# Kernel tuning notes

Hardware: AMD Instinct MI355X
Metric: run time of the kernel (lower is better)

The kernel has to match this reference:

```python
import jax, jax.numpy as jnp
import numpy as np

HID = 1024
NH = 4
DK = 256   # head_qk_dim
DV = 512   # head_v_dim
C = 64     # chunk size (fla default)
EPS = 1e-5
GLN = 16.0  # gate_logit_normalizer


def _xavier(key, shape, gain=2 ** (-2.5)):
    fan_in, fan_out = shape
    lim = gain * np.sqrt(6.0 / (fan_in + fan_out))
    return jax.random.uniform(key, shape, jnp.float32, -lim, lim)


def setup_inputs() -> dict:
    key = jax.random.key(0)
    ks = jax.random.split(key, 8)
    x = jax.random.normal(ks[0], (4, 2048, HID), jnp.float32)
    Wq = _xavier(ks[1], (HID, NH * DK))
    Wk = _xavier(ks[2], (HID, NH * DK))
    Wv = _xavier(ks[3], (HID, NH * DV))
    Wg = _xavier(ks[4], (HID, NH * DV))
    Wgk = _xavier(ks[5], (HID, NH))
    bgk = jnp.zeros((NH,), jnp.float32)
    Wo = _xavier(ks[6], (NH * DV, HID))
    gnorm_w = jnp.ones((DV,), jnp.float32)
    return {"x": x, "Wq": Wq, "Wk": Wk, "Wv": Wv, "Wg": Wg,
            "Wgk": Wgk, "bgk": bgk, "Wo": Wo, "gnorm_w": gnorm_w}


def _chunk_simple_gla(q, k, v, g):
    # q,k: [b,h,n,dk]; v: [b,h,n,dv]; g: [b,h,n] per-head scalar log-decay
    B, H, N, dk = q.shape
    dv = v.shape[-1]
    nc = N // C
    scale = dk ** -0.5
    q = q.reshape(B, H, nc, C, dk) * scale
    k = k.reshape(B, H, nc, C, dk)
    v = v.reshape(B, H, nc, C, dv)
    g = g.reshape(B, H, nc, C)
    gc = jnp.cumsum(g, axis=-1)          # inclusive within-chunk cumulative decay
    gt = gc[..., -1]                     # total chunk decay [b,h,nc]

    # intra-chunk: o[t] += sum_{s<=t} exp(gc_t - gc_s) (q_t.k_s) v_s
    dec = gc[..., :, None] - gc[..., None, :]              # [b,h,nc,C,C]
    mask = jnp.tril(jnp.ones((C, C), bool))
    A = jnp.einsum('bhntd,bhnsd->bhnts', q, k)
    A = A * jnp.where(mask, jnp.exp(jnp.where(mask, dec, 0.0)), 0.0)
    o_intra = jnp.einsum('bhnts,bhnsd->bhntd', A, v)

    # inter-chunk: carry state S [b,h,dk,dv] across chunks
    qs = jnp.moveaxis(q, 2, 0)
    ks_ = jnp.moveaxis(k, 2, 0)
    vs = jnp.moveaxis(v, 2, 0)
    gcs = jnp.moveaxis(gc, 2, 0)
    gts = jnp.moveaxis(gt, 2, 0)
    S0 = jnp.zeros((B, H, dk, dv), q.dtype)

    def step(S, inp):
        qc, kc, vc, gcc, gtc = inp
        o_int = jnp.einsum('bhtd,bhde->bhte', qc * jnp.exp(gcc)[..., None], S)
        kd = kc * jnp.exp(gtc[..., None] - gcc)[..., None]
        S = jnp.exp(gtc)[..., None, None] * S + jnp.einsum('bhtd,bhte->bhde', kd, vc)
        return S, o_int

    _, o_inter = jax.lax.scan(step, S0, (qs, ks_, vs, gcs, gts))
    o = o_intra + jnp.moveaxis(o_inter, 0, 2)
    return o.reshape(B, H, N, dv)


def reference(x, Wq, Wk, Wv, Wg, Wgk, bgk, Wo, gnorm_w):
    B, N, _ = x.shape
    q = (x @ Wq).reshape(B, N, NH, DK).transpose(0, 2, 1, 3)
    k = (x @ Wk).reshape(B, N, NH, DK).transpose(0, 2, 1, 3)
    v = (x @ Wv).reshape(B, N, NH, DV).transpose(0, 2, 1, 3)
    gk = (x @ Wgk + bgk).transpose(0, 2, 1)          # [b,h,n]
    gk = jax.nn.log_sigmoid(gk) / GLN
    o = _chunk_simple_gla(q, k, v, gk)               # [b,h,n,dv]
    o = o.transpose(0, 2, 1, 3)                      # [b,n,h,dv]
    g = (x @ Wg).reshape(B, N, NH, DV)
    # FusedRMSNormSwishGate: RMSNorm(o) * swish(g)
    on = o * jax.lax.rsqrt(jnp.mean(o * o, axis=-1, keepdims=True) + EPS) * gnorm_w
    o = on * (g * jax.nn.sigmoid(g))
    o = o.reshape(B, N, NH * DV)
    return o @ Wo
```

## Files before the change

### kernel.cpp

```cpp
#include <hip/hip_runtime.h>

constexpr int B_  = 4;
constexpr int N_  = 2048;
constexpr int HID_ = 1024;
constexpr int NH_ = 4;
constexpr int DK_ = 256;
constexpr int DV_ = 512;
constexpr int C_  = 64;
constexpr int NC_ = 32;
constexpr int M_  = B_ * N_;
constexpr int NSEG_ = 4;
constexpr int CSEG_ = NC_ / NSEG_;
constexpr int QW_ = 6144;

using ushort_t = unsigned short;
typedef __attribute__((ext_vector_type(8))) short bf16x8;
typedef __attribute__((ext_vector_type(4))) float f32x4;

__device__ __forceinline__ ushort_t f2bf(float f) {
  union { float fv; unsigned u; } v; v.fv = f;
  unsigned r = v.u + 0x7FFFu + ((v.u >> 16) & 1u);
  return (ushort_t)(r >> 16);
}
__device__ __forceinline__ float bf2f(ushort_t u) {
  union { unsigned u; float f; } v; v.u = ((unsigned)u) << 16; return v.f;
}

__device__ __forceinline__ void gload_lds16(const void* g, void* l) {
  __builtin_amdgcn_global_load_lds(
      (const __attribute__((address_space(1))) unsigned int*)g,
      (__attribute__((address_space(3))) unsigned int*)l, 16, 0, 0);
}

__device__ __forceinline__ f32x4 mfma16(bf16x8 a, bf16x8 b, f32x4 c) {
  return __builtin_amdgcn_mfma_f32_16x16x32_bf16(a, b, c, 0, 0, 0);
}

#define GSTAGE_A(G, Kd, kt32, dst)                                             \
  do {                                                                         \
    _Pragma("unroll")                                                          \
    for (int j = 0; j < 2; ++j) {                                              \
      const int cb = j * 8 + wave;                                  \
      const int srow = (cb * 64 + lane) >> 2;                      \
      gload_lds16((G) + (size_t)srow * (Kd) + (kt32) * 32 + kp,                \
                  (dst) + cb * 512);                                           \
    }                                                                          \
  } while (0)
#define GSTAGE_B(G, Kd, kt32, dst)                                             \
  do {                                                                         \
    const int cb = wave;                                             \
    const int srow = (cb * 64 + lane) >> 2;                        \
    gload_lds16((G) + (size_t)srow * (Kd) + (kt32) * 32 + kp,                  \
                (dst) + cb * 512);                                             \
  } while (0)

template<bool BF16OUT>
__global__ __launch_bounds__(512) void gemm_mfma(
    const ushort_t* __restrict__ A, const ushort_t* __restrict__ BT,
    void* __restrict__ CV, int N, int K) {
  __shared__ ushort_t Ah[3][256 * 32];
  __shared__ ushort_t Bh[3][128 * 32];
  const int tid = threadIdx.x;
  const int wave = tid >> 6, lane = tid & 63;
  const size_t brow = (size_t)blockIdx.y * 256;
  const size_t bcol = (size_t)blockIdx.x * 128;
  const int wr = (wave >> 1) * 64, wc = (wave & 1) * 64;
  const int frow = lane & 15;
  const int fko  = ((lane >> 4) ^ (frow & 3)) * 8;
  const int kp   = (((lane & 3) ^ ((lane >> 2) & 3)) * 8);

  f32x4 acc[4][4];
#pragma unroll
  for (int m = 0; m < 4; ++m)
#pragma unroll
    for (int n = 0; n < 4; ++n) acc[m][n] = f32x4{0.f, 0.f, 0.f, 0.f};

  const ushort_t* Ag = A + brow * K;
  const ushort_t* Bg = BT + bcol * K;
  const int NT = K >> 5;

  GSTAGE_A(Ag, K, 0, Ah[0]);
  GSTAGE_B(Bg, K, 0, Bh[0]);
  GSTAGE_A(Ag, K, 1, Ah[1]);
  GSTAGE_B(Bg, K, 1, Bh[1]);
  asm volatile("s_waitcnt vmcnt(3)" ::: "memory");
  __builtin_amdgcn_s_barrier();

  int rb = 0, sb = 2;
  bf16x8 af[4], bfr[4];
  for (int kt = 0; kt < NT; ++kt) {
#pragma unroll
    for (int m = 0; m < 4; ++m)
      af[m] = *(const bf16x8*)(&Ah[rb][(wr + m * 16 + frow) * 32 + fko]);
#pragma unroll
    for (int n = 0; n < 4; ++n)
      bfr[n] = *(const bf16x8*)(&Bh[rb][(wc + n * 16 + frow) * 32 + fko]);
    if (kt + 2 < NT) {
      GSTAGE_A(Ag, K, kt + 2, Ah[sb]);
      GSTAGE_B(Bg, K, kt + 2, Bh[sb]);
    }
#pragma unroll
    for (int m = 0; m < 4; ++m)
#pragma unroll
      for (int n = 0; n < 4; ++n) acc[m][n] = mfma16(af[m], bfr[n], acc[m][n]);
    if (kt + 1 < NT) {
      if (kt + 2 < NT) asm volatile("s_waitcnt vmcnt(3)" ::: "memory");
      else             asm volatile("s_waitcnt vmcnt(0)" ::: "memory");
      __builtin_amdgcn_s_barrier();
    }
    rb = (rb == 2) ? 0 : rb + 1;
    sb = (sb == 2) ? 0 : sb + 1;
  }

  const int crow = (lane >> 4) * 4;
  const int ccol = lane & 15;
#pragma unroll
  for (int m = 0; m < 4; ++m)
#pragma unroll
    for (int n = 0; n < 4; ++n) {
      const size_t base = (brow + wr + m * 16 + crow) * (size_t)N + (bcol + wc + n * 16 + ccol);
      if constexpr (BF16OUT) {
        ushort_t* Out = (ushort_t*)CV;
#pragma unroll
        for (int j = 0; j < 4; ++j) Out[base + (size_t)j * N] = f2bf(acc[m][n][j]);
      } else {
        float* Out = (float*)CV;
#pragma unroll
        for (int j = 0; j < 4; ++j) Out[base + (size_t)j * N] = acc[m][n][j];
      }
    }
}

__global__ __launch_bounds__(256) void prep_all(
    const float* __restrict__ Wq, const float* __restrict__ Wk,
    const float* __restrict__ Wv, const float* __restrict__ Wg,
    const float* __restrict__ Wo, const float* __restrict__ x,
    const float* __restrict__ Wgk, const float* __restrict__ bgk,
    ushort_t* __restrict__ WqT, ushort_t* __restrict__ WkT,
    ushort_t* __restrict__ WvT, ushort_t* __restrict__ WgT,
    ushort_t* __restrict__ WoT, ushort_t* __restrict__ xb,
    float* __restrict__ gkbuf) {
  __shared__ float tile[32][33];
  __shared__ float4 red4[256];
  const int blk = blockIdx.x;
  const int tid = threadIdx.x;
  if (blk >= 8192) {
    const int row = blk - 8192;
    const size_t i = ((size_t)row * 1024) + tid * 4;
    float4 v = *(const float4*)(x + i);
    ushort4 r;
    r.x = f2bf(v.x); r.y = f2bf(v.y); r.z = f2bf(v.z); r.w = f2bf(v.w);
    *(ushort4*)(xb + i) = r;
    float4 p = {0.f, 0.f, 0.f, 0.f};
    const float4* wg4 = (const float4*)Wgk;
    const float xv[4] = {v.x, v.y, v.z, v.w};
#pragma unroll
    for (int j = 0; j < 4; ++j) {
      float4 wg = wg4[tid * 4 + j];
      p.x += xv[j] * wg.x; p.y += xv[j] * wg.y;
      p.z += xv[j] * wg.z; p.w += xv[j] * wg.w;
    }
    red4[tid] = p;
    __syncthreads();
    for (int off2 = 128; off2; off2 >>= 1) {
      if (tid < off2) {
        float4 a = red4[tid], b4 = red4[tid + off2];
        a.x += b4.x; a.y += b4.y; a.z += b4.z; a.w += b4.w;
        red4[tid] = a;
      }
      __syncthreads();
    }
    if (tid < 4) {
      const float z  = (&red4[0].x)[tid] + bgk[tid];
      const float ls = fminf(z, 0.f) - log1pf(expf(-fabsf(z)));
      const int b = row >> 11, n = row & 2047;
      gkbuf[((size_t)(b * NH_ + tid)) * N_ + n] = ls * (1.0f / 16.0f);
    }
    return;
  }
  const float* W; ushort_t* WT; int K, Nn, gxw, local;
  if (blk < 1024)      { W = Wq; WT = WqT; K = 1024; Nn = 1024; gxw = 32; local = blk; }
  else if (blk < 2048) { W = Wk; WT = WkT; K = 1024; Nn = 1024; gxw = 32; local = blk - 1024; }
  else if (blk < 4096) { W = Wv; WT = WvT; K = 1024; Nn = 2048; gxw = 64; local = blk - 2048; }
  else if (blk < 6144) { W = Wg; WT = WgT; K = 1024; Nn = 2048; gxw = 64; local = blk - 4096; }
  else                 { W = Wo; WT = WoT; K = 2048; Nn = 1024; gxw = 32; local = blk - 6144; }
  const int n0 = (local % gxw) * 32, k0 = (local / gxw) * 32;
  const int tx = tid & 31, ty = tid >> 5;
#pragma unroll
  for (int i = 0; i < 32; i += 8)
    tile[ty + i][tx] = W[(size_t)(k0 + ty + i) * Nn + n0 + tx];
  __syncthreads();
#pragma unroll
  for (int i = 0; i < 32; i += 8)
    WT[(size_t)(n0 + ty + i) * K + k0 + tx] = f2bf(tile[tx][ty + i]);
}

__global__ __launch_bounds__(64) void cumsum_kernel(const float* __restrict__ gkbuf,
                                                    float* __restrict__ gcbuf) {
  const int bh = blockIdx.x;
  const int c  = threadIdx.x;
  if (c < NC_) {
    const size_t base = (size_t)bh * N_ + c * C_;
    float acc = 0.f;
    for (int t = 0; t < C_; ++t) { acc += gkbuf[base + t]; gcbuf[base + t] = acc; }
  }
}

__global__ __launch_bounds__(256) void post_qkv(
    const ushort_t* __restrict__ qkvg16, const float* __restrict__ gc,
    ushort_t* __restrict__ Abuf, ushort_t* __restrict__ kT,
    ushort_t* __restrict__ vT, ushort_t* __restrict__ q16) {
  __shared__ __align__(16) char smem[256 * 68 * 2 + 256];
  const int gblk = blockIdx.x;
  const int tid = threadIdx.x;

  if (gblk < 512) {
    const int blk = gblk;
    const int bh  = blk >> 5, c = blk & 31;
    const int b   = bh >> 2, h = bh & 3;
    float* gcs = (float*)smem;
    const int w = tid >> 6, l = tid & 63;
    const int frow = l & 15, fgrp = l >> 4;
    if (tid < 64) gcs[tid] = gc[(size_t)bh * N_ + c * C_ + tid];
    __syncthreads();

    const size_t rbase = (size_t)(b * N_ + c * C_);
    bf16x8 aqr[8];
#pragma unroll
    for (int kk = 0; kk < 8; ++kk)
      aqr[kk] = *(const bf16x8*)(qkvg16 + (rbase + w * 16 + frow) * QW_ +
                                 h * 256 + kk * 32 + fgrp * 8);

    ushort_t* ab = Abuf + (size_t)blk * 4096;
    const float scl = 0.0625f;
#pragma unroll
    for (int n = 0; n < 4; ++n) {
      f32x4 acc = f32x4{0.f, 0.f, 0.f, 0.f};
#pragma unroll
      for (int kk = 0; kk < 8; ++kk) {
        bf16x8 bk = *(const bf16x8*)(qkvg16 + (rbase + n * 16 + frow) * QW_ +
                                     1024 + h * 256 + kk * 32 + fgrp * 8);
        acc = mfma16(aqr[kk], bk, acc);
      }
      const int s = n * 16 + frow;
      const float gcss = gcs[s];
#pragma unroll
      for (int j = 0; j < 4; ++j) {
        const int t = w * 16 + fgrp * 4 + j;
        const float val = (s <= t) ? acc[j] * scl * expf(gcs[t] - gcss) : 0.f;
        ab[(size_t)t * 64 + s] = f2bf(val);
      }
    }
  } else if (gblk < 1024) {
    const int blk = gblk - 512;
    const int bh = blk >> 5, c = blk & 31;
    const int b = bh >> 2, h = bh & 3;
    ushort_t (*kl)[68] = (ushort_t (*)[68])smem;
    float* fk = (float*)(smem + 256 * 68 * 2);
    if (tid < 64) {
      const float gct = gc[(size_t)bh * N_ + c * C_ + tid];
      const float gt  = gc[(size_t)bh * N_ + c * C_ + 63];
      fk[tid] = expf(gt - gct);
    }
    __syncthreads();
    const ushort_t* kb = qkvg16 + (size_t)(b * N_ + c * C_) * QW_ + 1024 + h * 256;
    for (int it = 0; it < 8; ++it) {
      const int e = it * 256 + tid;
      const int t = e >> 5, d8 = (e & 31) * 8;
      bf16x8 kv = *(const bf16x8*)(kb + (size_t)t * QW_ + d8);
      const float f = fk[t];
#pragma unroll
      for (int j = 0; j < 8; ++j) kl[d8 + j][t] = f2bf(bf2f((ushort_t)kv[j]) * f);
    }
    __syncthreads();
    ushort_t* out = kT + (size_t)blk * 16384;
    for (int it = 0; it < 8; ++it) {
      const int e = it * 256 + tid;
      const int d = e >> 3, t8 = (e & 7) * 8;
      ushort4 lo, hi;
      lo.x = kl[d][t8 + 0]; lo.y = kl[d][t8 + 1]; lo.z = kl[d][t8 + 2]; lo.w = kl[d][t8 + 3];
      hi.x = kl[d][t8 + 4]; hi.y = kl[d][t8 + 5]; hi.z = kl[d][t8 + 6]; hi.w = kl[d][t8 + 7];
      *(ushort4*)(out + (size_t)d * 64 + t8)     = lo;
      *(ushort4*)(out + (size_t)d * 64 + t8 + 4) = hi;
    }
  } else if (gblk < 2048) {
    const int blk = gblk - 1024;
    const int eh = blk & 1, c = (blk >> 1) & 31, bh = blk >> 6;
    const int b = bh >> 2, h = bh & 3;
    ushort_t (*vl)[68] = (ushort_t (*)[68])smem;
    const ushort_t* vb = qkvg16 + (size_t)(b * N_ + c * C_) * QW_ + 2048 + h * 512 + eh * 256;
    for (int it = 0; it < 8; ++it) {
      const int e = it * 256 + tid;
      const int s = e >> 5, c8 = (e & 31) * 8;
      bf16x8 val = *(const bf16x8*)(vb + (size_t)s * QW_ + c8);
#pragma unroll
      for (int j = 0; j < 8; ++j) vl[c8 + j][s] = (ushort_t)val[j];
    }
    __syncthreads();
    ushort_t* out = vT + (size_t)bh * 512 * 2048 + (size_t)(eh * 256) * 2048 + c * C_;
    for (int it = 0; it < 8; ++it) {
      const int e = it * 256 + tid;
      const int r = e >> 3, t8 = (e & 7) * 8;
      ushort4 lo, hi;
      lo.x = vl[r][t8 + 0]; lo.y = vl[r][t8 + 1]; lo.z = vl[r][t8 + 2]; lo.w = vl[r][t8 + 3];
      hi.x = vl[r][t8 + 4]; hi.y = vl[r][t8 + 5]; hi.z = vl[r][t8 + 6]; hi.w = vl[r][t8 + 7];
      *(ushort4*)(out + (size_t)r * 2048 + t8)     = lo;
      *(ushort4*)(out + (size_t)r * 2048 + t8 + 4) = hi;
    }
  } else {
    const size_t i8 = ((size_t)(gblk - 2048) * 256 + tid) * 8;
    const int row = (int)(i8 >> 10);
    const int col = (int)(i8 & 1023);
    const int b = row >> 11, n = row & 2047;
    const int h = col >> 8;
    const float f = 0.0625f * expf(gc[(size_t)(b * NH_ + h) * N_ + n]);
    bf16x8 v = *(const bf16x8*)(qkvg16 + (size_t)row * QW_ + col);
    ushort_t r[8];
#pragma unroll
    for (int j = 0; j < 8; ++j) r[j] = f2bf(bf2f((ushort_t)v[j]) * f);
    *(bf16x8*)(q16 + i8) = *(bf16x8*)r;
  }
}

#define LOAD_AQ(cc, dst)                                                       \
  do {                                                                         \
    _Pragma("unroll")                                                          \
    for (int kk = 0; kk < 8; ++kk)                                             \
      dst[kk] = *(const bf16x8*)(qbase + (size_t)((cc) * C_ + w * 16 + frow) * 1024 + \
                                 kk * 32 + fgrp * 8);                          \
  } while (0)
#define LOAD_BV(cc, dst)                                                       \
  do {                                                                         \
    _Pragma("unroll")                                                          \
    for (int kt = 0; kt < 2; ++kt)                                             \
      _Pragma("unroll")                                                        \
      for (int n = 0; n < 4; ++n)                                              \
        dst[kt][n] = *(const bf16x8*)(vbase + (size_t)(n * 16 + frow) * 2048 + \
                                      (cc) * C_ + kt * 32 + fgrp * 8);         \
  } while (0)
#define LOAD_AA(cc, dst)                                                       \
  do {                                                                         \
    _Pragma("unroll")                                                          \
    for (int kt = 0; kt < 2; ++kt)                                             \
      dst[kt] = *(const bf16x8*)(abase + (size_t)(cc) * 4096 +                 \
                                 (w * 16 + frow) * 64 + kt * 32 + fgrp * 8);   \
  } while (0)

__global__ __launch_bounds__(256) void scan_mfma(
    const ushort_t* __restrict__ q16,
    const ushort_t* __restrict__ kT,
    const ushort_t* __restrict__ vT,
    const ushort_t* __restrict__ ab,
    const float*    __restrict__ gc,
    ushort_t* __restrict__ o,
    float*    __restrict__ U) {
  const int bh = blockIdx.x, vblk = blockIdx.y, sg = blockIdx.z;
  const int b = bh >> 2, h = bh & 3;
  const int e0 = vblk * 64;
  const int c0 = sg * CSEG_;
  __shared__ ushort_t sbt[64][264];
  __shared__ float egts[NC_];
  const int tid = threadIdx.x;
  const int w = tid >> 6, l = tid & 63;
  const int frow = l & 15, fgrp = l >> 4;

  for (int i = tid; i < 64 * 264 / 2; i += 256) ((unsigned*)&sbt[0][0])[i] = 0u;
  if (tid < NC_) egts[tid] = expf(gc[(size_t)bh * N_ + tid * C_ + 63]);
  f32x4 s_acc[4][4];
#pragma unroll
  for (int sm = 0; sm < 4; ++sm)
#pragma unroll
    for (int sn = 0; sn < 4; ++sn) s_acc[sm][sn] = f32x4{0.f, 0.f, 0.f, 0.f};
  __syncthreads();

  const ushort_t* qbase = q16 + (size_t)(b * N_) * 1024 + h * 256;
  const ushort_t* kbase = kT + (size_t)bh * NC_ * 16384;
  const ushort_t* vbase = vT + (size_t)bh * 512 * 2048 + (size_t)e0 * 2048;
  const ushort_t* abase = ab + (size_t)bh * NC_ * 4096;
  ushort_t*       obase = o + (size_t)(b * N_) * 2048 + h * 512 + e0;

  bf16x8 aqP[8], bvP[2][4], aaP[2];
  LOAD_AQ(c0, aqP);
  LOAD_BV(c0, bvP);
  LOAD_AA(c0, aaP);

  for (int c = c0; c < c0 + CSEG_; ++c) {
    const float egt = egts[c];

    bf16x8 aq[8], bv[2][4], aa[2];
#pragma unroll
    for (int kk = 0; kk < 8; ++kk) aq[kk] = aqP[kk];
#pragma unroll
    for (int kt = 0; kt < 2; ++kt) {
      aa[kt] = aaP[kt];
#pragma unroll
      for (int n = 0; n < 4; ++n) bv[kt][n] = bvP[kt][n];
    }

#pragma unroll
    for (int n = 0; n < 4; ++n) {
      f32x4 oa = f32x4{0.f, 0.f, 0.f, 0.f};
#pragma unroll
      for (int kt = 0; kt < 2; ++kt) oa = mfma16(aa[kt], bv[kt][n], oa);
#pragma unroll
      for (int kk = 0; kk < 8; ++kk) {
        bf16x8 bs = *(const bf16x8*)(&sbt[n * 16 + frow][kk * 32 + fgrp * 8]);
        oa = mfma16(aq[kk], bs, oa);
      }
#pragma unroll
      for (int j = 0; j < 4; ++j)
        obase[(size_t)(c * C_ + w * 16 + fgrp * 4 + j) * 2048 + n * 16 + frow] = f2bf(oa[j]);
    }

#pragma unroll
    for (int sm = 0; sm < 4; ++sm)
#pragma unroll
      for (int sn = 0; sn < 4; ++sn)
#pragma unroll
        for (int j = 0; j < 4; ++j) s_acc[sm][sn][j] *= egt;
#pragma unroll
    for (int kt = 0; kt < 2; ++kt)
#pragma unroll
      for (int sm = 0; sm < 4; ++sm) {
        bf16x8 ak = *(const bf16x8*)(kbase + (size_t)c * 16384 +
                                     (size_t)(w * 64 + sm * 16 + frow) * 64 + kt * 32 + fgrp * 8);
#pragma unroll
        for (int sn = 0; sn < 4; ++sn)
          s_acc[sm][sn] = mfma16(ak, bv[kt][sn], s_acc[sm][sn]);
      }

    if (c + 1 < c0 + CSEG_) {
      LOAD_AQ(c + 1, aqP);
      LOAD_BV(c + 1, bvP);
      LOAD_AA(c + 1, aaP);
    }

    __syncthreads();

#pragma unroll
    for (int sm = 0; sm < 4; ++sm)
#pragma unroll
      for (int sn = 0; sn < 4; ++sn) {
        ushort4 pk;
        pk.x = f2bf(s_acc[sm][sn][0]); pk.y = f2bf(s_acc[sm][sn][1]);
        pk.z = f2bf(s_acc[sm][sn][2]); pk.w = f2bf(s_acc[sm][sn][3]);
        *(ushort4*)&sbt[sn * 16 + frow][w * 64 + sm * 16 + fgrp * 4] = pk;
      }
    __syncthreads();
  }

  if (sg < NSEG_ - 1) {
    float* ub = U + (size_t)(bh * (NSEG_ - 1) + sg) * 256 * 512;
#pragma unroll
    for (int sm = 0; sm < 4; ++sm)
#pragma unroll
      for (int sn = 0; sn < 4; ++sn)
#pragma unroll
        for (int j = 0; j < 4; ++j)
          ub[(size_t)(w * 64 + sm * 16 + fgrp * 4 + j) * 512 + e0 + sn * 16 + frow] =
              s_acc[sm][sn][j];
  }
}

__global__ __launch_bounds__(256) void correct_kernel(
    const ushort_t* __restrict__ q16, const float* __restrict__ U,
    const float* __restrict__ gc, ushort_t* __restrict__ o) {
  const int bh = blockIdx.x, vb = blockIdx.y, z = blockIdx.z;
  const int sg = z + 1, c0 = sg * CSEG_;
  const int b = bh >> 2, h = bh & 3;
  __shared__ ushort_t sT[16][264];
  __shared__ float dseg[CSEG_];
  const int tid = threadIdx.x;
  const int w = tid >> 6, l = tid & 63;
  const int frow = l & 15, fgrp = l >> 4;

  {
    const int e = tid >> 4, dbase = (tid & 15) * 16;
    float E[NSEG_ - 1];
#pragma unroll
    for (int s = 0; s < NSEG_ - 1; ++s) {
      float gsum = 0.f;
      for (int c = s * CSEG_; c < (s + 1) * CSEG_; ++c)
        gsum += gc[(size_t)bh * N_ + c * C_ + 63];
      E[s] = expf(gsum);
    }
#pragma unroll
    for (int d = 0; d < 16; ++d) {
      float S = 0.f;
      for (int s = 0; s <= z; ++s)
        S = E[s] * S + U[(size_t)(bh * (NSEG_ - 1) + s) * 256 * 512 +
                         (size_t)(dbase + d) * 512 + vb * 16 + e];
      sT[e][dbase + d] = f2bf(S);
    }
  }
  if (tid < CSEG_) {
    float s = 0.f;
    for (int i = 0; i < tid; ++i) s += gc[(size_t)bh * N_ + (c0 + i) * C_ + 63];
    dseg[tid] = expf(s);
  }
  __syncthreads();

  const ushort_t* qbase = q16 + (size_t)(b * N_) * 1024 + h * 256;
  ushort_t* obase = o + (size_t)(b * N_) * 2048 + h * 512 + vb * 16;

  for (int c = c0; c < c0 + CSEG_; ++c) {
    const float D = dseg[c - c0];
    f32x4 oa = f32x4{0.f, 0.f, 0.f, 0.f};
#pragma unroll
    for (int kk = 0; kk < 8; ++kk) {
      bf16x8 aq = *(const bf16x8*)(qbase + (size_t)(c * C_ + w * 16 + frow) * 1024 + kk * 32 + fgrp * 8);
      bf16x8 bs = *(const bf16x8*)(&sT[frow][kk * 32 + fgrp * 8]);
      oa = mfma16(aq, bs, oa);
    }
#pragma unroll
    for (int j = 0; j < 4; ++j) {
      const size_t idx = (size_t)(c * C_ + w * 16 + fgrp * 4 + j) * 2048 + frow;
      obase[idx] = f2bf(bf2f(obase[idx]) + D * oa[j]);
    }
  }
}

__global__ __launch_bounds__(256) void normgate_kernel(const ushort_t* __restrict__ o,
    const ushort_t* __restrict__ qkvg16, const float* __restrict__ w,
    ushort_t* __restrict__ ob) {
  const int blk = blockIdx.x;
  const int row = blk >> 2, h = blk & 3;
  const size_t base = (size_t)blk * DV_;
  const size_t gbase = (size_t)row * QW_ + 4096 + h * DV_;
  const int tid = threadIdx.x;
  __shared__ float red2[256];
  const float v0 = bf2f(o[base + tid]), v1 = bf2f(o[base + tid + 256]);
  red2[tid] = v0 * v0 + v1 * v1;
  __syncthreads();
  for (int off = 128; off; off >>= 1) {
    if (tid < off) red2[tid] += red2[tid + off];
    __syncthreads();
  }
  const float rms = rsqrtf(red2[0] * (1.0f / 512.0f) + 1e-5f);
  const float g0 = bf2f(qkvg16[gbase + tid]), g1 = bf2f(qkvg16[gbase + tid + 256]);
  const float sw0 = g0 / (1.f + expf(-g0));
  const float sw1 = g1 / (1.f + expf(-g1));
  ob[base + tid]       = f2bf(v0 * rms * w[tid] * sw0);
  ob[base + tid + 256] = f2bf(v1 * rms * w[tid + 256] * sw1);
}

extern "C" void kernel_launch(void* const* d_in, const int* in_sizes, int n_in,
                              void* d_out, int out_size, void* d_ws, size_t ws_size,
                              hipStream_t stream) {
  (void)in_sizes; (void)n_in; (void)out_size; (void)ws_size;
  const float* x    = (const float*)d_in[0];
  const float* Wq   = (const float*)d_in[1];
  const float* Wk   = (const float*)d_in[2];
  const float* Wv   = (const float*)d_in[3];
  const float* Wg   = (const float*)d_in[4];
  const float* Wgk  = (const float*)d_in[5];
  const float* bgk  = (const float*)d_in[6];
  const float* Wo   = (const float*)d_in[7];
  const float* gw   = (const float*)d_in[8];

  float* ws = (float*)d_ws;
  size_t off = 0;
  float* gk = ws + off; off += (size_t)16 * N_;
  float* gc = ws + off; off += (size_t)16 * N_;
  ushort_t* qkvg16 = (ushort_t*)(ws + off); off += (size_t)M_ * QW_ / 2;
  ushort_t* o    = (ushort_t*)(ws + off); off += (size_t)M_ * 2048 / 2;
  ushort_t* ab16 = (ushort_t*)(ws + off); off += (size_t)16 * NC_ * 4096 / 2;
  ushort_t* q16  = (ushort_t*)(ws + off); off += (size_t)M_ * 1024 / 2;
  ushort_t* kTp  = (ushort_t*)(ws + off); off += (size_t)16 * NC_ * 16384 / 2;
  ushort_t* vTp  = (ushort_t*)(ws + off); size_t vTp_off = off; off += (size_t)16 * 512 * 2048 / 2;
  ushort_t* xb   = (ushort_t*)(ws + off); size_t xb_off = off; off += (size_t)M_ * HID_ / 2;
  ushort_t* WqT  = (ushort_t*)(ws + off); off += (size_t)1024 * 1024 / 2;
  ushort_t* WkT  = (ushort_t*)(ws + off); off += (size_t)1024 * 1024 / 2;
  ushort_t* WvT  = (ushort_t*)(ws + off); off += (size_t)2048 * 1024 / 2;
  ushort_t* WgT  = (ushort_t*)(ws + off); off += (size_t)2048 * 1024 / 2;
  ushort_t* WoT  = (ushort_t*)(ws + off); off += (size_t)1024 * 2048 / 2;
  float*    U    = ws + xb_off;
  ushort_t* ob   = (ushort_t*)(ws + vTp_off);

  dim3 thr(256);
  prep_all<<<16384, thr, 0, stream>>>(Wq, Wk, Wv, Wg, Wo, x, Wgk, bgk,
                                      WqT, WkT, WvT, WgT, WoT, xb, gk);

  gemm_mfma<true><<<dim3(48, 32), 512, 0, stream>>>(xb, WqT, qkvg16, QW_, 1024);
  cumsum_kernel<<<16, 64, 0, stream>>>(gk, gc);
  post_qkv<<<6144, thr, 0, stream>>>(qkvg16, gc, ab16, kTp, vTp, q16);
  scan_mfma<<<dim3(16, 8, NSEG_), thr, 0, stream>>>(q16, kTp, vTp, ab16, gc, o, U);
  correct_kernel<<<dim3(16, 32, NSEG_ - 1), thr, 0, stream>>>(q16, U, gc, o);
  normgate_kernel<<<M_ * NH_, thr, 0, stream>>>(o, qkvg16, gw, ob);
  gemm_mfma<false><<<dim3(8, 32), 512, 0, stream>>>(ob, WoT, (float*)d_out, 1024, 2048);
}
```

Before: 383.0 us.

## Use 256x256-tile MFMA GEMM for QKVG projection and raise MFMA priority

Adds a new GEMM kernel with 256x256 block tiles (8 waves, each computing 128x64) for the large fused QKVG projection. It replaces the 128-column-tile launch, halving the number of blocks and doubling operand reuse per LDS load. It also wraps the MFMA loops in s_setprio to favour issue of matrix instructions over other waves' loads. The bigger tile roughly doubles LDS per block and raises accumulator register count, which may lower occupancy. With 768 blocks on 256 CUs the tail balance changes.

```diff
diff --git a/kernel.cpp b/kernel.cpp
--- a/kernel.cpp
+++ b/kernel.cpp
@@ -99,10 +99,12 @@
       GSTAGE_A(Ag, K, kt + 2, Ah[sb]);
       GSTAGE_B(Bg, K, kt + 2, Bh[sb]);
     }
+    __builtin_amdgcn_s_setprio(1);
 #pragma unroll
     for (int m = 0; m < 4; ++m)
 #pragma unroll
       for (int n = 0; n < 4; ++n) acc[m][n] = mfma16(af[m], bfr[n], acc[m][n]);
+    __builtin_amdgcn_s_setprio(0);
     if (kt + 1 < NT) {
       if (kt + 2 < NT) asm volatile("s_waitcnt vmcnt(3)" ::: "memory");
       else             asm volatile("s_waitcnt vmcnt(0)" ::: "memory");
@@ -128,6 +130,89 @@
 #pragma unroll
         for (int j = 0; j < 4; ++j) Out[base + (size_t)j * N] = acc[m][n][j];
       }
+    }
+}
+
+#define GSTAGE256(G, Kd, kt32, dst)                                            \
+  do {                                                                         \
+    _Pragma("unroll")                                                          \
+    for (int j = 0; j < 2; ++j) {                                              \
+      const int cb = j * 8 + wave;                                  \
+      const int srow = (cb * 64 + lane) >> 2;                      \
+      gload_lds16((G) + (size_t)srow * (Kd) + (kt32) * 32 + kp,                \
+                  (dst) + cb * 512);                                           \
+    }                                                                          \
+  } while (0)
+
+__global__ __launch_bounds__(512) void gemm_mfma256(
+    const ushort_t* __restrict__ A, const ushort_t* __restrict__ BT,
+    ushort_t* __restrict__ C, int N, int K) {
+  __shared__ ushort_t Ah[3][256 * 32];
+  __shared__ ushort_t Bh[3][256 * 32];
+  const int tid = threadIdx.x;
+  const int wave = tid >> 6, lane = tid & 63;
+  const size_t brow = (size_t)blockIdx.y * 256;
+  const size_t bcol = (size_t)blockIdx.x * 256;
+  const int wrow = (wave >> 2) * 128;
+  const int wcol = (wave & 3) * 64;
+  const int frow = lane & 15;
+  const int fko  = ((lane >> 4) ^ (frow & 3)) * 8;
+  const int kp   = (((lane & 3) ^ ((lane >> 2) & 3)) * 8);
+
+  f32x4 acc[8][4];
+#pragma unroll
+  for (int m = 0; m < 8; ++m)
+#pragma unroll
+    for (int n = 0; n < 4; ++n) acc[m][n] = f32x4{0.f, 0.f, 0.f, 0.f};
+
+  const ushort_t* Ag = A + brow * K;
+  const ushort_t* Bg = BT + bcol * K;
+  const int NT = K >> 5;
+
+  GSTAGE256(Ag, K, 0, Ah[0]);
+  GSTAGE256(Bg, K, 0, Bh[0]);
+  GSTAGE256(Ag, K, 1, Ah[1]);
+  GSTAGE256(Bg, K, 1, Bh[1]);
+  asm volatile("s_waitcnt vmcnt(4)" ::: "memory");
+  __builtin_amdgcn_s_barrier();
+
+  int rb = 0, sb = 2;
+  bf16x8 af[8], bfr[4];
+  for (int kt = 0; kt < NT; ++kt) {
+#pragma unroll
+    for (int m = 0; m < 8; ++m)
+      af[m] = *(const bf16x8*)(&Ah[rb][(wrow + m * 16 + frow) * 32 + fko]);
+#pragma unroll
+    for (int n = 0; n < 4; ++n)
+      bfr[n] = *(const bf16x8*)(&Bh[rb][(wcol + n * 16 + frow) * 32 + fko]);
+    if (kt + 2 < NT) {
+      GSTAGE256(Ag, K, kt + 2, Ah[sb]);
+      GSTAGE256(Bg, K, kt + 2, Bh[sb]);
+    }
+    __builtin_amdgcn_s_setprio(1);
+#pragma unroll
+    for (int m = 0; m < 8; ++m)
+#pragma unroll
+      for (int n = 0; n < 4; ++n) acc[m][n] = mfma16(af[m], bfr[n], acc[m][n]);
+    __builtin_amdgcn_s_setprio(0);
+    if (kt + 1 < NT) {
+      if (kt + 2 < NT) asm volatile("s_waitcnt vmcnt(4)" ::: "memory");
+      else             asm volatile("s_waitcnt vmcnt(0)" ::: "memory");
+      __builtin_amdgcn_s_barrier();
+    }
+    rb = (rb == 2) ? 0 : rb + 1;
+    sb = (sb == 2) ? 0 : sb + 1;
+  }
+
+  const int crow = (lane >> 4) * 4;
+  const int ccol = lane & 15;
+#pragma unroll
+  for (int m = 0; m < 8; ++m)
+#pragma unroll
+    for (int n = 0; n < 4; ++n) {
+      const size_t base = (brow + wrow + m * 16 + crow) * (size_t)N + (bcol + wcol + n * 16 + ccol);
+#pragma unroll
+      for (int j = 0; j < 4; ++j) C[base + (size_t)j * N] = f2bf(acc[m][n][j]);
     }
 }
 
@@ -581,7 +666,7 @@
   prep_all<<<16384, thr, 0, stream>>>(Wq, Wk, Wv, Wg, Wo, x, Wgk, bgk,
                                       WqT, WkT, WvT, WgT, WoT, xb, gk);
 
-  gemm_mfma<true><<<dim3(48, 32), 512, 0, stream>>>(xb, WqT, qkvg16, QW_, 1024);
+  gemm_mfma256<<<dim3(24, 32), 512, 0, stream>>>(xb, WqT, qkvg16, QW_, 1024);
   cumsum_kernel<<<16, 64, 0, stream>>>(gk, gc);
   post_qkv<<<6144, thr, 0, stream>>>(qkvg16, gc, ab16, kTp, vTp, q16);
   scan_mfma<<<dim3(16, 8, NSEG_), thr, 0, stream>>>(q16, kTp, vTp, ab16, gc, o, U);
```

Measured after the change: 381.6 us. About the same (-0.4%).
